# Optimization experiments

Measured on AMD Instinct MI355X. Metric: run time of the kernel, lower is better.

## Reference

```python
import jax, jax.numpy as jnp
import numpy as np

B, S, V, D, H, L, FF = 2, 1024, 32000, 512, 8, 4, 2048
DK = D // H
WIN, GLOB = 128, 16
EPS = 1e-5


def setup_inputs() -> dict:
    key = jax.random.key(0)
    ks = jax.random.split(key, 12)
    def rn(k, shape, s=0.02):
        return jax.random.normal(k, shape, jnp.float32) * s
    ln2 = jnp.stack([jnp.ones((L, 2, D)), jnp.zeros((L, 2, D))], axis=2)   # [L, 2 norms, (scale,bias), D]
    ln3 = jnp.stack([jnp.ones((L, 3, D)), jnp.zeros((L, 3, D))], axis=2)   # [L, 3 norms, (scale,bias), D]
    fln = jnp.stack([jnp.ones((D,)), jnp.zeros((D,))], axis=0)             # [(scale,bias), D]
    return {
        "src": jax.random.randint(ks[0], (B, S), 0, V),
        "tgt": jax.random.randint(ks[1], (B, S), 0, V),
        "enc_embed": rn(ks[2], (V, D)),
        "dec_embed": rn(ks[3], (V, D)),
        "enc_attn_w": rn(ks[4], (L, 4, D, D)),   # q,k,v,o projections
        "enc_attn_b": jnp.zeros((L, 4, D)),
        "enc_ln": ln2,
        "enc_ffn_w1": rn(ks[5], (L, D, FF)),
        "enc_ffn_b1": jnp.zeros((L, FF)),
        "enc_ffn_w2": rn(ks[6], (L, FF, D)),
        "enc_ffn_b2": jnp.zeros((L, D)),
        "enc_final_ln": fln,
        "dec_attn_w": rn(ks[7], (L, 8, D, D)),   # self q,k,v,o then cross q,k,v,o
        "dec_attn_b": jnp.zeros((L, 8, D)),
        "dec_ln": ln3,
        "dec_ffn_w1": rn(ks[8], (L, D, FF)),
        "dec_ffn_b1": jnp.zeros((L, FF)),
        "dec_ffn_w2": rn(ks[9], (L, FF, D)),
        "dec_ffn_b2": jnp.zeros((L, D)),
        "dec_final_ln": fln,
        "out_w": rn(ks[10], (D, V)),
        "out_b": jnp.zeros((V,)),
    }


def _ln(x, p):
    m = jnp.mean(x, -1, keepdims=True)
    v = jnp.var(x, -1, keepdims=True)
    return p[0] * (x - m) * jax.lax.rsqrt(v + EPS) + p[1]


def _rope(x):
    # x: [B, H, S, DK]; half-split rotary embedding
    half = DK // 2
    pos = jnp.arange(x.shape[2], dtype=jnp.float32)
    inv = 1.0 / (10000.0 ** (jnp.arange(half, dtype=jnp.float32) / half))
    ang = pos[:, None] * inv[None, :]                   # [S, half]
    c, s = jnp.cos(ang), jnp.sin(ang)
    x1, x2 = x[..., :half], x[..., half:]
    return jnp.concatenate([x1 * c - x2 * s, x1 * s + x2 * c], axis=-1)


def _mask(n, causal):
    # local sliding window + global tokens, optional causal
    i = jnp.arange(n)[:, None]
    j = jnp.arange(n)[None, :]
    allowed = jnp.abs(i - j) <= WIN
    allowed = allowed | (i < GLOB) | (j < GLOB)
    if causal:
        allowed = allowed & (j <= i)
    return allowed


def _attn(q_in, k_in, v_in, w, b, causal):
    # w: [4, D, D] (q,k,v,o), b: [4, D]
    def heads(x, idx):
        y = x @ w[idx] + b[idx]
        return y.reshape(x.shape[0], x.shape[1], H, DK).transpose(0, 2, 1, 3)  # [B,H,S,DK]
    Q, K, Vh = heads(q_in, 0), heads(k_in, 1), heads(v_in, 2)
    Q, K = _rope(Q), _rope(K)
    scores = jnp.einsum('bhqd,bhkd->bhqk', Q, K) / np.sqrt(DK).astype(np.float32)
    scores = jnp.where(_mask(q_in.shape[1], causal)[None, None], scores, -1e9)
    A = jax.nn.softmax(scores, axis=-1)
    o = jnp.einsum('bhqk,bhkd->bhqd', A, Vh).transpose(0, 2, 1, 3).reshape(q_in.shape[0], q_in.shape[1], D)
    return o @ w[3] + b[3]


def _ffn(x, w1, b1, w2, b2):
    return jax.nn.gelu(x @ w1 + b1) @ w2 + b2


def _forward(src, tgt, enc_embed, dec_embed, enc_attn_w, enc_attn_b, enc_ln,
             enc_ffn_w1, enc_ffn_b1, enc_ffn_w2, enc_ffn_b2, enc_final_ln,
             dec_attn_w, dec_attn_b, dec_ln, dec_ffn_w1, dec_ffn_b1,
             dec_ffn_w2, dec_ffn_b2, dec_final_ln, out_w, out_b):
    sqrt_d = np.sqrt(D).astype(np.float32)
    # encoder
    x = enc_embed[src] * sqrt_d
    for l in range(L):
        n = _ln(x, enc_ln[l, 0])
        x = x + _attn(n, n, n, enc_attn_w[l], enc_attn_b[l], False)
        n = _ln(x, enc_ln[l, 1])
        x = x + _ffn(n, enc_ffn_w1[l], enc_ffn_b1[l], enc_ffn_w2[l], enc_ffn_b2[l])
    mem = _ln(x, enc_final_ln)
    # decoder
    y = dec_embed[tgt] * sqrt_d
    for l in range(L):
        n = _ln(y, dec_ln[l, 0])
        y = y + _attn(n, n, n, dec_attn_w[l, :4], dec_attn_b[l, :4], True)
        n = _ln(y, dec_ln[l, 1])
        y = y + _attn(n, mem, mem, dec_attn_w[l, 4:], dec_attn_b[l, 4:], False)
        n = _ln(y, dec_ln[l, 2])
        y = y + _ffn(n, dec_ffn_w1[l], dec_ffn_b1[l], dec_ffn_w2[l], dec_ffn_b2[l])
    y = _ln(y, dec_final_ln)
    return y @ out_w + out_b


def reference(src, tgt, enc_embed, dec_embed, enc_attn_w, enc_attn_b, enc_ln,
              enc_ffn_w1, enc_ffn_b1, enc_ffn_w2, enc_ffn_b2, enc_final_ln,
              dec_attn_w, dec_attn_b, dec_ln, dec_ffn_w1, dec_ffn_b1,
              dec_ffn_w2, dec_ffn_b2, dec_final_ln, out_w, out_b):
    return _forward(src, tgt, enc_embed, dec_embed, enc_attn_w, enc_attn_b, enc_ln,
                    enc_ffn_w1, enc_ffn_b1, enc_ffn_w2, enc_ffn_b2, enc_final_ln,
                    dec_attn_w, dec_attn_b, dec_ln, dec_ffn_w1, dec_ffn_b1,
                    dec_ffn_w2, dec_ffn_b2, dec_final_ln, out_w, out_b)
```

## Files before the change

kernel.cpp:

```cpp
#include <hip/hip_runtime.h>
#include <cstdint>
#include <cstddef>

#define S_LEN 1024
#define DM 512
#define NHEAD 8
#define HDIM 64
#define NLAYER 4
#define FFD 2048
#define VOC 32000
#define WINSZ 128
#define GLOBSZ 16

using half8 = __attribute__((ext_vector_type(8))) _Float16;
using f32x4 = __attribute__((ext_vector_type(4))) float;

static __device__ __forceinline__ f32x4 mfma16(half8 a, half8 b, f32x4 c) {
  return __builtin_amdgcn_mfma_f32_16x16x32_f16(a, b, c, 0, 0, 0);
}

typedef __attribute__((address_space(1))) const void gvoid;
typedef __attribute__((address_space(3))) void lvoid;
static __device__ __forceinline__ void gload16(const void* g, void* l) {
  __builtin_amdgcn_global_load_lds((gvoid*)g, (lvoid*)l, 16, 0, 0);
}
template <int N>
static __device__ __forceinline__ void waitv() {
  asm volatile("s_waitcnt vmcnt(%0)" :: "i"(N) : "memory");
}

__global__ __launch_bounds__(256) void transpose_k(const float* __restrict__ in,
                                                   _Float16* __restrict__ out,
                                                   int R, int C)
{
  __shared__ float t[32][33];
  const float* ip = in + (size_t)blockIdx.z * R * C;
  _Float16* op = out + (size_t)blockIdx.z * R * C;
  int c0 = blockIdx.x * 32, r0 = blockIdx.y * 32;
  int tx = threadIdx.x & 31, ty = threadIdx.x >> 5;
#pragma unroll
  for (int i = 0; i < 32; i += 8)
    t[ty + i][tx] = ip[(size_t)(r0 + ty + i) * C + c0 + tx];
  __syncthreads();
#pragma unroll
  for (int i = 0; i < 32; i += 8)
    op[(size_t)(c0 + ty + i) * R + r0 + tx] = (_Float16)t[tx][ty + i];
}

__global__ __launch_bounds__(256) void embed2_k(const int* __restrict__ src,
                                                const int* __restrict__ tgt,
                                                const float* __restrict__ enc_embed,
                                                const float* __restrict__ dec_embed,
                                                const float* __restrict__ enc_ln0,
                                                const float* __restrict__ dec_ln0,
                                                float* __restrict__ xbuf,
                                                float* __restrict__ ybuf,
                                                _Float16* __restrict__ nbuf,
                                                _Float16* __restrict__ nbuf2)
{
  int which = blockIdx.y;
  const int* ids = which ? tgt : src;
  const float* emb = which ? dec_embed : enc_embed;
  const float* gamma = which ? dec_ln0 : enc_ln0;
  const float* beta = gamma + 512;
  float* xout = which ? ybuf : xbuf;
  _Float16* nout = which ? nbuf2 : nbuf;

  int row = blockIdx.x * 4 + (threadIdx.x >> 6);
  int lane = threadIdx.x & 63;
  const float* er = emb + (size_t)ids[row] * DM + lane * 8;
  float4 v0 = *(const float4*)er;
  float4 v1 = *(const float4*)(er + 4);
  float vals[8] = {v0.x, v0.y, v0.z, v0.w, v1.x, v1.y, v1.z, v1.w};
  float s = 0.f, ss = 0.f;
#pragma unroll
  for (int j = 0; j < 8; ++j) {
    vals[j] *= 22.627416997969522f;
    s += vals[j]; ss += vals[j] * vals[j];
  }
#pragma unroll
  for (int m = 1; m < 64; m <<= 1) { s += __shfl_xor(s, m); ss += __shfl_xor(ss, m); }
  float mean = s * (1.f / 512.f);
  float var = ss * (1.f / 512.f) - mean * mean;
  float rstd = rsqrtf(var + 1e-5f);
  float* xr = xout + (size_t)row * DM + lane * 8;
  _Float16* orow = nout + (size_t)row * DM + lane * 8;
  const float* gp = gamma + lane * 8;
  const float* bp = beta + lane * 8;
#pragma unroll
  for (int j = 0; j < 8; ++j) {
    xr[j] = vals[j];
    orow[j] = (_Float16)(gp[j] * (vals[j] - mean) * rstd + bp[j]);
  }
}

__global__ __launch_bounds__(256) void ln_k(const float* __restrict__ x,
                                            const float* __restrict__ gamma,
                                            const float* __restrict__ beta,
                                            _Float16* __restrict__ outp)
{
  int row = blockIdx.x * 4 + (threadIdx.x >> 6);
  int lane = threadIdx.x & 63;
  const float* xr = x + (size_t)row * DM + lane * 8;
  float4 v0 = *(const float4*)xr;
  float4 v1 = *(const float4*)(xr + 4);
  float vals[8] = {v0.x, v0.y, v0.z, v0.w, v1.x, v1.y, v1.z, v1.w};
  float s = 0.f, ss = 0.f;
#pragma unroll
  for (int j = 0; j < 8; ++j) { s += vals[j]; ss += vals[j] * vals[j]; }
#pragma unroll
  for (int m = 1; m < 64; m <<= 1) { s += __shfl_xor(s, m); ss += __shfl_xor(ss, m); }
  float mean = s * (1.f / 512.f);
  float var = ss * (1.f / 512.f) - mean * mean;
  float rstd = rsqrtf(var + 1e-5f);
  _Float16* orow = outp + (size_t)row * DM + lane * 8;
  const float* gp = gamma + lane * 8;
  const float* bp = beta + lane * 8;
#pragma unroll
  for (int j = 0; j < 8; ++j)
    orow[j] = (_Float16)(gp[j] * (vals[j] - mean) * rstd + bp[j]);
}

template <int BM, int BN, int EPI, int MODE, bool WIDE = (MODE != 0)>
__global__ __launch_bounds__(256) void gemm_k(const _Float16* __restrict__ A,
                                              const _Float16* __restrict__ B,
                                              const float* __restrict__ bias,
                                              const float* __restrict__ resid,
                                              void* __restrict__ Cout,
                                              _Float16* __restrict__ vtout,
                                              int M, int N, int K)
{
  constexpr int WAVE_M = WIDE ? BM / 4 : BM / 2;
  constexpr int WAVE_N = WIDE ? BN : BN / 2;
  constexpr int FMW = WAVE_M / 16;
  constexpr int FNW = WAVE_N / 16;
  constexpr int LPS = BM / 32 + BN / 32;
  static_assert(MODE == 0 || (WIDE && BN == 64), "rope modes need 64-col waves");

  __shared__ __align__(16) _Float16 As[3][BM * 64];
  __shared__ __align__(16) _Float16 Bs[3][BN * 64];
  const int tid = threadIdx.x;
  const int lane = tid & 63, wid = tid >> 6;
  const int g = lane >> 4, ql = lane & 15;

  const int gx = gridDim.x;
  const int nwg = gx * gridDim.y;
  const int orig = blockIdx.y * gx + blockIdx.x;
  const int q = nwg >> 3, r = nwg & 7;
  const int xcd = orig & 7, rest = orig >> 3;
  const int id = (xcd < r ? xcd * (q + 1) : r * (q + 1) + (xcd - r) * q) + rest;
  const int bm = (id % gx) * BM, bn = (id / gx) * BN;
  const int wm = WIDE ? wid * WAVE_M : (wid >> 1) * WAVE_M;
  const int wn = WIDE ? 0 : (wid & 1) * WAVE_N;

  const _Float16* Bp;
  if constexpr (MODE == 2) {
    int srcrow0 = ((bn >> 10) * 8 + 5 + ((bn >> 9) & 1)) * 512 + (bn & 511);
    Bp = B + (size_t)srcrow0 * K;
  } else {
    Bp = B + (size_t)bn * K;
  }

  f32x4 acc[FMW][FNW];
#pragma unroll
  for (int a = 0; a < FMW; ++a)
#pragma unroll
    for (int b = 0; b < FNW; ++b) acc[a][b] = f32x4{0.f, 0.f, 0.f, 0.f};

  auto stage = [&](int buf, int kt) {
#pragma unroll
    for (int r2 = 0; r2 < BM / 32; ++r2) {
      int off = r2 * 4096 + tid * 16;
      int row = off >> 7, slot = (off >> 4) & 7;
      gload16(A + (size_t)(bm + row) * K + kt + ((slot ^ (row & 7)) << 3),
              (char*)&As[buf][0] + r2 * 4096 + wid * 1024);
    }
#pragma unroll
    for (int r2 = 0; r2 < BN / 32; ++r2) {
      int off = r2 * 4096 + tid * 16;
      int row = off >> 7, slot = (off >> 4) & 7;
      gload16(Bp + (size_t)row * K + kt + ((slot ^ (row & 7)) << 3),
              (char*)&Bs[buf][0] + r2 * 4096 + wid * 1024);
    }
  };

  auto compute = [&](int cur) {
#pragma unroll
    for (int kk = 0; kk < 2; ++kk) {
      half8 af[FMW], bf[FNW];
#pragma unroll
      for (int a = 0; a < FMW; ++a) {
        int row = wm + a * 16 + ql;
        af[a] = *(const half8*)((const char*)&As[cur][0] + row * 128 + (((kk * 4 + g) ^ (row & 7)) << 4));
      }
#pragma unroll
      for (int b = 0; b < FNW; ++b) {
        int row = wn + b * 16 + ql;
        bf[b] = *(const half8*)((const char*)&Bs[cur][0] + row * 128 + (((kk * 4 + g) ^ (row & 7)) << 4));
      }
      __builtin_amdgcn_s_setprio(1);
#pragma unroll
      for (int a = 0; a < FMW; ++a)
#pragma unroll
        for (int b = 0; b < FNW; ++b) acc[a][b] = mfma16(af[a], bf[b], acc[a][b]);
      __builtin_amdgcn_s_setprio(0);
    }
  };

  const int nk = K >> 6;
  stage(0, 0);
  stage(1, 64);
  for (int t = 0; t < nk; ++t) {
    if (t + 1 < nk) waitv<LPS>(); else waitv<0>();
    __builtin_amdgcn_s_barrier();
    __builtin_amdgcn_sched_barrier(0);
    if (t + 2 < nk) stage((t + 2) % 3, (t + 2) << 6);
    compute(t % 3);
  }

#pragma unroll
  for (int a = 0; a < FMW; ++a) {
    const int row0 = bm + wm + a * 16 + g * 4;
    float v[FNW][4];
#pragma unroll
    for (int b2 = 0; b2 < FNW; ++b2) {
      int col = bn + wn + b2 * 16 + ql;
      float bv;
      if constexpr (MODE == 2) {
        int bcol = ((col >> 10) * 8 + 5 + ((col >> 9) & 1)) * 512 + (col & 511);
        bv = bias[bcol];
      } else {
        bv = bias[col];
      }
#pragma unroll
      for (int r2 = 0; r2 < 4; ++r2) v[b2][r2] = acc[a][b2][r2] + bv;
    }
    if constexpr (MODE != 0) {
      const int seg = bn >> 9;
      bool dorope = (MODE == 3) || (MODE == 1 && seg < 2) ||
                    (MODE == 2 && ((bn >> 9) & 1) == 0);
      if (dorope) {
        const float scale = (MODE == 3 || (MODE == 1 && seg == 0)) ? 0.125f : 1.0f;
#pragma unroll
        for (int b2 = 0; b2 < 2; ++b2) {
          int d = b2 * 16 + ql;
          float inv = __expf(-(float)d * 0.28782313662425574f);
#pragma unroll
          for (int r2 = 0; r2 < 4; ++r2) {
            float sp = (float)((row0 & 1023) + r2);
            float sn, cs; __sincosf(sp * inv, &sn, &cs);
            float x1 = v[b2][r2], x2 = v[b2 + 2][r2];
            v[b2][r2]     = (x1 * cs - x2 * sn) * scale;
            v[b2 + 2][r2] = (x1 * sn + x2 * cs) * scale;
          }
        }
      }
    }
#pragma unroll
    for (int b2 = 0; b2 < FNW; ++b2) {
      int col = bn + wn + b2 * 16 + ql;
      if constexpr (MODE == 1) {
        if (col < 1024) {
#pragma unroll
          for (int r2 = 0; r2 < 4; ++r2)
            ((_Float16*)Cout)[(size_t)(row0 + r2) * 1024 + col] = (_Float16)v[b2][r2];
        } else {
          int rowidx = ((row0 >> 10) << 9) + (col - 1024);
          union { _Float16 h[4]; uint2 u; } pk;
#pragma unroll
          for (int r2 = 0; r2 < 4; ++r2) pk.h[r2] = (_Float16)v[b2][r2];
          *(uint2*)&vtout[((size_t)rowidx << 10) + (row0 & 1023)] = pk.u;
        }
      } else if constexpr (MODE == 2) {
        if ((col & 1023) < 512) {
#pragma unroll
          for (int r2 = 0; r2 < 4; ++r2)
            ((_Float16*)Cout)[(size_t)(row0 + r2) * 2048 + ((col >> 10) << 9) + (col & 511)] = (_Float16)v[b2][r2];
        } else {
          int rowidx = (col & ~1023) + ((row0 >> 10) << 9) + (col & 511);
          union { _Float16 h[4]; uint2 u; } pk;
#pragma unroll
          for (int r2 = 0; r2 < 4; ++r2) pk.h[r2] = (_Float16)v[b2][r2];
          *(uint2*)&vtout[((size_t)rowidx << 10) + (row0 & 1023)] = pk.u;
        }
      } else {
#pragma unroll
        for (int r2 = 0; r2 < 4; ++r2) {
          float x = v[b2][r2];
          if constexpr (EPI == 1) {
            float u = x;
            x = u / (1.f + __expf(-1.5957691216057308f * (u + 0.044715f * u * u * u)));
          }
          if constexpr (EPI == 2) x += resid[(size_t)(row0 + r2) * N + col];
          if constexpr (EPI == 0 || EPI == 1)
            ((_Float16*)Cout)[(size_t)(row0 + r2) * N + col] = (_Float16)x;
          else if constexpr (EPI == 2)
            ((float*)Cout)[(size_t)(row0 + r2) * N + col] = x;
          else
            __builtin_nontemporal_store(x, &((float*)Cout)[(size_t)(row0 + r2) * N + col]);
        }
      }
    }
  }
}

template <bool CAUSAL>
__global__ __launch_bounds__(256) void attn_k(const _Float16* __restrict__ qb, int qs, int qoff,
                                              const _Float16* __restrict__ kb, int ks, int koff,
                                              const _Float16* __restrict__ vt,
                                              _Float16* __restrict__ out)
{
  __shared__ _Float16 plds[4][16 * 40];
  const int bh = blockIdx.y, b = bh >> 3, h = bh & 7;
  const int wid = threadIdx.x >> 6, lane = threadIdx.x & 63;
  const int g = lane >> 4, ql = lane & 15;
  const int q0 = blockIdx.x * 64 + wid * 16;
  const size_t rb = (size_t)b * S_LEN;

  half8 qf0, qf1;
  {
    const _Float16* qp = qb + (rb + q0 + ql) * qs + qoff + h * HDIM + g * 8;
    qf0 = *(const half8*)qp;
    qf1 = *(const half8*)(qp + 32);
  }
  float mrun[4] = {-1e30f, -1e30f, -1e30f, -1e30f};
  float srun[4] = {0.f, 0.f, 0.f, 0.f};
  f32x4 oacc[4];
#pragma unroll
  for (int c = 0; c < 4; ++c) oacc[c] = f32x4{0.f, 0.f, 0.f, 0.f};

  const _Float16* vbase = vt + (((size_t)(b * 512 + h * HDIM)) << 10);
  _Float16* pw = plds[wid];

  auto proc = [&](int k0) {
    const _Float16* kp = kb + (rb + k0 + ql) * ks + koff + h * HDIM + g * 8;
    half8 kf00 = *(const half8*)kp;
    half8 kf01 = *(const half8*)(kp + 32);
    half8 kf10 = *(const half8*)(kp + (size_t)16 * ks);
    half8 kf11 = *(const half8*)(kp + (size_t)16 * ks + 32);

    f32x4 s0 = f32x4{0.f, 0.f, 0.f, 0.f};
    f32x4 s1 = f32x4{0.f, 0.f, 0.f, 0.f};
    __builtin_amdgcn_s_setprio(1);
    s0 = mfma16(qf0, kf00, s0); s0 = mfma16(qf1, kf01, s0);
    s1 = mfma16(qf0, kf10, s1); s1 = mfma16(qf1, kf11, s1);
    __builtin_amdgcn_s_setprio(0);

    float p0[4], p1[4];
#pragma unroll
    for (int r = 0; r < 4; ++r) {
      int i = q0 + 4 * g + r;
      int j0 = k0 + ql, j1 = j0 + 16;
      float a0 = s0[r], a1 = s1[r];
      int d0 = i - j0, d1 = i - j1;
      bool ok0 = (d0 <= WINSZ && d0 >= -WINSZ) || (i < GLOBSZ) || (j0 < GLOBSZ);
      bool ok1 = (d1 <= WINSZ && d1 >= -WINSZ) || (i < GLOBSZ) || (j1 < GLOBSZ);
      if (CAUSAL) { ok0 = ok0 && (j0 <= i); ok1 = ok1 && (j1 <= i); }
      a0 = ok0 ? a0 : -1e9f;
      a1 = ok1 ? a1 : -1e9f;
      float mx = fmaxf(a0, a1);
      mx = fmaxf(mx, __shfl_xor(mx, 1));
      mx = fmaxf(mx, __shfl_xor(mx, 2));
      mx = fmaxf(mx, __shfl_xor(mx, 4));
      mx = fmaxf(mx, __shfl_xor(mx, 8));
      float mnew = fmaxf(mrun[r], mx);
      float alpha = __expf(mrun[r] - mnew);
      float e0 = __expf(a0 - mnew), e1 = __expf(a1 - mnew);
      float ps = e0 + e1;
      ps += __shfl_xor(ps, 1);
      ps += __shfl_xor(ps, 2);
      ps += __shfl_xor(ps, 4);
      ps += __shfl_xor(ps, 8);
      srun[r] = srun[r] * alpha + ps;
      mrun[r] = mnew;
#pragma unroll
      for (int c = 0; c < 4; ++c) oacc[c][r] *= alpha;
      p0[r] = e0; p1[r] = e1;
    }
#pragma unroll
    for (int r = 0; r < 4; ++r) {
      pw[(4 * g + r) * 40 + ql] = (_Float16)p0[r];
      pw[(4 * g + r) * 40 + 16 + ql] = (_Float16)p1[r];
    }
    half8 pa = *(const half8*)&pw[ql * 40 + g * 8];
    __builtin_amdgcn_s_setprio(1);
#pragma unroll
    for (int c = 0; c < 4; ++c) {
      half8 vf = *(const half8*)(vbase + (((size_t)(16 * c + ql)) << 10) + k0 + 8 * g);
      oacc[c] = mfma16(pa, vf, oacc[c]);
    }
    __builtin_amdgcn_s_setprio(0);
  };

  const int kend = CAUSAL ? (q0 + 16) : S_LEN;
  int lo = 0, hi = kend;
  if (q0 >= GLOBSZ) {
    lo = (q0 - WINSZ) & ~31;
    if (lo < 0) lo = 0;
    if (!CAUSAL) {
      int h2 = q0 + 16 + WINSZ;
      hi = (h2 < kend) ? h2 : kend;
    }
  }
  if (lo > 0) proc(0);
  for (int k0 = lo; k0 < hi; k0 += 32) proc(k0);

#pragma unroll
  for (int c = 0; c < 4; ++c)
#pragma unroll
    for (int r = 0; r < 4; ++r) {
      float val = oacc[c][r] / srun[r];
      out[(rb + q0 + 4 * g + r) * DM + h * HDIM + 16 * c + ql] = (_Float16)val;
    }
}

extern "C" void kernel_launch(void* const* d_in, const int* in_sizes, int n_in,
                              void* d_out, int out_size, void* d_ws, size_t ws_size,
                              hipStream_t stream)
{
  const int*   src         = (const int*)d_in[0];
  const int*   tgt         = (const int*)d_in[1];
  const float* enc_embed   = (const float*)d_in[2];
  const float* dec_embed   = (const float*)d_in[3];
  const float* enc_attn_w  = (const float*)d_in[4];
  const float* enc_attn_b  = (const float*)d_in[5];
  const float* enc_ln      = (const float*)d_in[6];
  const float* enc_ffn_w1  = (const float*)d_in[7];
  const float* enc_ffn_b1  = (const float*)d_in[8];
  const float* enc_ffn_w2  = (const float*)d_in[9];
  const float* enc_ffn_b2  = (const float*)d_in[10];
  const float* enc_fln     = (const float*)d_in[11];
  const float* dec_attn_w  = (const float*)d_in[12];
  const float* dec_attn_b  = (const float*)d_in[13];
  const float* dec_ln      = (const float*)d_in[14];
  const float* dec_ffn_w1  = (const float*)d_in[15];
  const float* dec_ffn_b1  = (const float*)d_in[16];
  const float* dec_ffn_w2  = (const float*)d_in[17];
  const float* dec_ffn_b2  = (const float*)d_in[18];
  const float* dec_fln     = (const float*)d_in[19];
  const float* out_w       = (const float*)d_in[20];
  const float* out_b       = (const float*)d_in[21];
  float* logits = (float*)d_out;

  char* wsp = (char*)d_ws;
  size_t off = 0;
  auto alloc = [&](size_t bytes) -> void* {
    void* p = wsp + off;
    off += (bytes + 255) & ~(size_t)255;
    return p;
  };
  _Float16* enc_attn_wt = (_Float16*)alloc((size_t)16 * 512 * 512 * 2);
  _Float16* dec_attn_wt = (_Float16*)alloc((size_t)32 * 512 * 512 * 2);
  _Float16* e_ffn1_wt   = (_Float16*)alloc((size_t)4 * 2048 * 512 * 2);
  _Float16* e_ffn2_wt   = (_Float16*)alloc((size_t)4 * 2048 * 512 * 2);
  _Float16* d_ffn1_wt   = (_Float16*)alloc((size_t)4 * 2048 * 512 * 2);
  _Float16* d_ffn2_wt   = (_Float16*)alloc((size_t)4 * 2048 * 512 * 2);
  _Float16* out_wt      = (_Float16*)alloc((size_t)VOC * 512 * 2);
  float*    xbuf        = (float*)alloc((size_t)2048 * 512 * 4);
  float*    ybuf        = (float*)alloc((size_t)2048 * 512 * 4);
  _Float16* nbuf        = (_Float16*)alloc((size_t)2048 * 512 * 2);
  _Float16* nbuf2       = (_Float16*)alloc((size_t)2048 * 512 * 2);
  _Float16* qkvb        = (_Float16*)alloc((size_t)2048 * 1024 * 2);
  _Float16* aob         = (_Float16*)alloc((size_t)2048 * 512 * 2);
  _Float16* hbuf        = (_Float16*)alloc((size_t)2048 * 2048 * 2);
  _Float16* memb        = (_Float16*)alloc((size_t)2048 * 512 * 2);
  _Float16* cqb         = (_Float16*)alloc((size_t)2048 * 512 * 2);
  _Float16* ckvb        = (_Float16*)alloc((size_t)2048 * 2048 * 2);
  _Float16* vts         = (_Float16*)alloc((size_t)2 * 512 * 1024 * 2);
  _Float16* vtc         = (_Float16*)alloc((size_t)8 * 512 * 1024 * 2);

  transpose_k<<<dim3(16, 16, 16), 256, 0, stream>>>(enc_attn_w, enc_attn_wt, 512, 512);
  transpose_k<<<dim3(16, 16, 32), 256, 0, stream>>>(dec_attn_w, dec_attn_wt, 512, 512);
  transpose_k<<<dim3(64, 16, 4), 256, 0, stream>>>(enc_ffn_w1, e_ffn1_wt, 512, 2048);
  transpose_k<<<dim3(16, 64, 4), 256, 0, stream>>>(enc_ffn_w2, e_ffn2_wt, 2048, 512);
  transpose_k<<<dim3(64, 16, 4), 256, 0, stream>>>(dec_ffn_w1, d_ffn1_wt, 512, 2048);
  transpose_k<<<dim3(16, 64, 4), 256, 0, stream>>>(dec_ffn_w2, d_ffn2_wt, 2048, 512);
  transpose_k<<<dim3(1000, 16, 1), 256, 0, stream>>>(out_w, out_wt, 512, VOC);

  embed2_k<<<dim3(512, 2), 256, 0, stream>>>(src, tgt, enc_embed, dec_embed,
                                             enc_ln, dec_ln, xbuf, ybuf, nbuf, nbuf2);

  for (int l = 0; l < NLAYER; ++l) {
    const float* g0 = enc_ln + ((size_t)(l * 2 + 0) * 2 + 0) * 512;
    if (l > 0) ln_k<<<512, 256, 0, stream>>>(xbuf, g0, g0 + 512, nbuf);
    gemm_k<64, 64, 0, 1><<<dim3(32, 24), 256, 0, stream>>>(
        nbuf, enc_attn_wt + (size_t)l * 4 * 262144,
        enc_attn_b + (size_t)l * 4 * 512, nullptr, qkvb, vts, 2048, 1536, 512);
    attn_k<false><<<dim3(16, 16), 256, 0, stream>>>(qkvb, 1024, 0, qkvb, 1024, 512, vts, aob);
    gemm_k<64, 32, 2, 0><<<dim3(32, 16), 256, 0, stream>>>(
        aob, enc_attn_wt + (size_t)(l * 4 + 3) * 262144,
        enc_attn_b + (size_t)(l * 4 + 3) * 512, xbuf, xbuf, nullptr, 2048, 512, 512);
    const float* g1 = enc_ln + ((size_t)(l * 2 + 1) * 2 + 0) * 512;
    ln_k<<<512, 256, 0, stream>>>(xbuf, g1, g1 + 512, nbuf);
    gemm_k<64, 64, 1, 0><<<dim3(32, 32), 256, 0, stream>>>(
        nbuf, e_ffn1_wt + (size_t)l * 2048 * 512,
        enc_ffn_b1 + (size_t)l * 2048, nullptr, hbuf, nullptr, 2048, 2048, 512);
    gemm_k<64, 32, 2, 0><<<dim3(32, 16), 256, 0, stream>>>(
        hbuf, e_ffn2_wt + (size_t)l * 512 * 2048,
        enc_ffn_b2 + (size_t)l * 512, xbuf, xbuf, nullptr, 2048, 512, 2048);
  }
  ln_k<<<512, 256, 0, stream>>>(xbuf, enc_fln, enc_fln + 512, memb);

  gemm_k<64, 64, 0, 2><<<dim3(32, 64), 256, 0, stream>>>(
      memb, dec_attn_wt, dec_attn_b, nullptr, ckvb, vtc, 2048, 4096, 512);

  for (int l = 0; l < NLAYER; ++l) {
    const float* g0 = dec_ln + ((size_t)(l * 3 + 0) * 2 + 0) * 512;
    const _Float16* dn = (l == 0) ? nbuf2 : nbuf;
    if (l > 0) ln_k<<<512, 256, 0, stream>>>(ybuf, g0, g0 + 512, nbuf);
    gemm_k<64, 64, 0, 1><<<dim3(32, 24), 256, 0, stream>>>(
        dn, dec_attn_wt + (size_t)l * 8 * 262144,
        dec_attn_b + (size_t)l * 8 * 512, nullptr, qkvb, vts, 2048, 1536, 512);
    attn_k<true><<<dim3(16, 16), 256, 0, stream>>>(qkvb, 1024, 0, qkvb, 1024, 512, vts, aob);
    gemm_k<64, 32, 2, 0><<<dim3(32, 16), 256, 0, stream>>>(
        aob, dec_attn_wt + (size_t)(l * 8 + 3) * 262144,
        dec_attn_b + (size_t)(l * 8 + 3) * 512, ybuf, ybuf, nullptr, 2048, 512, 512);
    const float* g1 = dec_ln + ((size_t)(l * 3 + 1) * 2 + 0) * 512;
    ln_k<<<512, 256, 0, stream>>>(ybuf, g1, g1 + 512, nbuf);
    gemm_k<64, 64, 0, 3><<<dim3(32, 8), 256, 0, stream>>>(
        nbuf, dec_attn_wt + (size_t)(l * 8 + 4) * 262144,
        dec_attn_b + (size_t)(l * 8 + 4) * 512, nullptr, cqb, nullptr, 2048, 512, 512);
    attn_k<false><<<dim3(16, 16), 256, 0, stream>>>(cqb, 512, 0, ckvb, 2048, l * 512,
                                                    vtc + ((size_t)l << 20), aob);
    gemm_k<64, 32, 2, 0><<<dim3(32, 16), 256, 0, stream>>>(
        aob, dec_attn_wt + (size_t)(l * 8 + 7) * 262144,
        dec_attn_b + (size_t)(l * 8 + 7) * 512, ybuf, ybuf, nullptr, 2048, 512, 512);
    const float* g2 = dec_ln + ((size_t)(l * 3 + 2) * 2 + 0) * 512;
    ln_k<<<512, 256, 0, stream>>>(ybuf, g2, g2 + 512, nbuf);
    gemm_k<64, 64, 1, 0><<<dim3(32, 32), 256, 0, stream>>>(
        nbuf, d_ffn1_wt + (size_t)l * 2048 * 512,
        dec_ffn_b1 + (size_t)l * 2048, nullptr, hbuf, nullptr, 2048, 2048, 512);
    gemm_k<64, 32, 2, 0><<<dim3(32, 16), 256, 0, stream>>>(
        hbuf, d_ffn2_wt + (size_t)l * 512 * 2048,
        dec_ffn_b2 + (size_t)l * 512, ybuf, ybuf, nullptr, 2048, 512, 2048);
  }

  ln_k<<<512, 256, 0, stream>>>(ybuf, dec_fln, dec_fln + 512, nbuf);
  gemm_k<128, 64, 3, 0><<<dim3(16, 500), 256, 0, stream>>>(
      nbuf, out_wt, out_b, nullptr, logits, nullptr, 2048, VOC, 512);
}
```

Baseline: 1.203 ms.

## Merge weight transposes, retune GEMM swizzle/scheduling, and halve attention block size

```diff
diff --git a/kernel.cpp b/kernel.cpp
--- a/kernel.cpp
+++ b/kernel.cpp
@@ -29,13 +29,18 @@
   asm volatile("s_waitcnt vmcnt(%0)" :: "i"(N) : "memory");
 }
 
-__global__ __launch_bounds__(256) void transpose_k(const float* __restrict__ in,
-                                                   _Float16* __restrict__ out,
-                                                   int R, int C)
+__global__ __launch_bounds__(256) void transpose2_k(const float* __restrict__ inA,
+                                                    const float* __restrict__ inB,
+                                                    _Float16* __restrict__ outA,
+                                                    _Float16* __restrict__ outB,
+                                                    int R, int C, int splitZ)
 {
   __shared__ float t[32][33];
-  const float* ip = in + (size_t)blockIdx.z * R * C;
-  _Float16* op = out + (size_t)blockIdx.z * R * C;
+  int z = blockIdx.z;
+  const float* ip;
+  _Float16* op;
+  if (z < splitZ) { ip = inA + (size_t)z * R * C; op = outA + (size_t)z * R * C; }
+  else { ip = inB + (size_t)(z - splitZ) * R * C; op = outB + (size_t)(z - splitZ) * R * C; }
   int c0 = blockIdx.x * 32, r0 = blockIdx.y * 32;
   int tx = threadIdx.x & 31, ty = threadIdx.x >> 5;
 #pragma unroll
@@ -121,7 +126,7 @@
     orow[j] = (_Float16)(gp[j] * (vals[j] - mean) * rstd + bp[j]);
 }
 
-template <int BM, int BN, int EPI, int MODE, bool WIDE = (MODE != 0)>
+template <int BM, int BN, int EPI, int MODE, bool SWZ = false, bool NT = false>
 __global__ __launch_bounds__(256) void gemm_k(const _Float16* __restrict__ A,
                                               const _Float16* __restrict__ B,
                                               const float* __restrict__ bias,
@@ -130,10 +135,11 @@
                                               _Float16* __restrict__ vtout,
                                               int M, int N, int K)
 {
+  constexpr bool WIDE = (BN >= 64);
   constexpr int WAVE_M = WIDE ? BM / 4 : BM / 2;
   constexpr int WAVE_N = WIDE ? BN : BN / 2;
   constexpr int FMW = WAVE_M / 16;
-  constexpr int FNW = WAVE_N / 16;
+  constexpr int FNW = WIDE ? BN / 16 : BN / 32;
   constexpr int LPS = BM / 32 + BN / 32;
   static_assert(MODE == 0 || (WIDE && BN == 64), "rope modes need 64-col waves");
 
@@ -143,13 +149,18 @@
   const int lane = tid & 63, wid = tid >> 6;
   const int g = lane >> 4, ql = lane & 15;
 
-  const int gx = gridDim.x;
-  const int nwg = gx * gridDim.y;
-  const int orig = blockIdx.y * gx + blockIdx.x;
-  const int q = nwg >> 3, r = nwg & 7;
-  const int xcd = orig & 7, rest = orig >> 3;
-  const int id = (xcd < r ? xcd * (q + 1) : r * (q + 1) + (xcd - r) * q) + rest;
-  const int bm = (id % gx) * BM, bn = (id / gx) * BN;
+  int bm, bn;
+  if constexpr (SWZ) {
+    const int gx = gridDim.x;
+    const int nwg = gx * gridDim.y;
+    const int orig = blockIdx.y * gx + blockIdx.x;
+    const int q = nwg >> 3, r = nwg & 7;
+    const int xcd = orig & 7, rest = orig >> 3;
+    const int id = (xcd < r ? xcd * (q + 1) : r * (q + 1) + (xcd - r) * q) + rest;
+    bm = (id % gx) * BM; bn = (id / gx) * BN;
+  } else {
+    bm = blockIdx.x * BM; bn = blockIdx.y * BN;
+  }
   const int wm = WIDE ? wid * WAVE_M : (wid >> 1) * WAVE_M;
   const int wn = WIDE ? 0 : (wid & 1) * WAVE_N;
 
@@ -198,12 +209,10 @@
         int row = wn + b * 16 + ql;
         bf[b] = *(const half8*)((const char*)&Bs[cur][0] + row * 128 + (((kk * 4 + g) ^ (row & 7)) << 4));
       }
-      __builtin_amdgcn_s_setprio(1);
 #pragma unroll
       for (int a = 0; a < FMW; ++a)
 #pragma unroll
         for (int b = 0; b < FNW; ++b) acc[a][b] = mfma16(af[a], bf[b], acc[a][b]);
-      __builtin_amdgcn_s_setprio(0);
     }
   };
 
@@ -214,8 +223,8 @@
     if (t + 1 < nk) waitv<LPS>(); else waitv<0>();
     __builtin_amdgcn_s_barrier();
     __builtin_amdgcn_sched_barrier(0);
+    compute(t % 3);
     if (t + 2 < nk) stage((t + 2) % 3, (t + 2) << 6);
-    compute(t % 3);
   }
 
 #pragma unroll
@@ -294,10 +303,10 @@
           if constexpr (EPI == 2) x += resid[(size_t)(row0 + r2) * N + col];
           if constexpr (EPI == 0 || EPI == 1)
             ((_Float16*)Cout)[(size_t)(row0 + r2) * N + col] = (_Float16)x;
-          else if constexpr (EPI == 2)
+          else if constexpr (NT)
+            __builtin_nontemporal_store(x, &((float*)Cout)[(size_t)(row0 + r2) * N + col]);
+          else
             ((float*)Cout)[(size_t)(row0 + r2) * N + col] = x;
-          else
-            __builtin_nontemporal_store(x, &((float*)Cout)[(size_t)(row0 + r2) * N + col]);
         }
       }
     }
@@ -305,16 +314,16 @@
 }
 
 template <bool CAUSAL>
-__global__ __launch_bounds__(256) void attn_k(const _Float16* __restrict__ qb, int qs, int qoff,
+__global__ __launch_bounds__(128) void attn_k(const _Float16* __restrict__ qb, int qs, int qoff,
                                               const _Float16* __restrict__ kb, int ks, int koff,
                                               const _Float16* __restrict__ vt,
                                               _Float16* __restrict__ out)
 {
-  __shared__ _Float16 plds[4][16 * 40];
+  __shared__ _Float16 plds[2][16 * 40];
   const int bh = blockIdx.y, b = bh >> 3, h = bh & 7;
   const int wid = threadIdx.x >> 6, lane = threadIdx.x & 63;
   const int g = lane >> 4, ql = lane & 15;
-  const int q0 = blockIdx.x * 64 + wid * 16;
+  const int q0 = blockIdx.x * 32 + wid * 16;
   const size_t rb = (size_t)b * S_LEN;
 
   half8 qf0, qf1;
@@ -341,10 +350,8 @@
 
     f32x4 s0 = f32x4{0.f, 0.f, 0.f, 0.f};
     f32x4 s1 = f32x4{0.f, 0.f, 0.f, 0.f};
-    __builtin_amdgcn_s_setprio(1);
     s0 = mfma16(qf0, kf00, s0); s0 = mfma16(qf1, kf01, s0);
     s1 = mfma16(qf0, kf10, s1); s1 = mfma16(qf1, kf11, s1);
-    __builtin_amdgcn_s_setprio(0);
 
     float p0[4], p1[4];
 #pragma unroll
@@ -383,13 +390,11 @@
       pw[(4 * g + r) * 40 + 16 + ql] = (_Float16)p1[r];
     }
     half8 pa = *(const half8*)&pw[ql * 40 + g * 8];
-    __builtin_amdgcn_s_setprio(1);
 #pragma unroll
     for (int c = 0; c < 4; ++c) {
       half8 vf = *(const half8*)(vbase + (((size_t)(16 * c + ql)) << 10) + k0 + 8 * g);
       oacc[c] = mfma16(pa, vf, oacc[c]);
     }
-    __builtin_amdgcn_s_setprio(0);
   };
 
   const int kend = CAUSAL ? (q0 + 16) : S_LEN;
@@ -469,13 +474,13 @@
   _Float16* vts         = (_Float16*)alloc((size_t)2 * 512 * 1024 * 2);
   _Float16* vtc         = (_Float16*)alloc((size_t)8 * 512 * 1024 * 2);
 
-  transpose_k<<<dim3(16, 16, 16), 256, 0, stream>>>(enc_attn_w, enc_attn_wt, 512, 512);
-  transpose_k<<<dim3(16, 16, 32), 256, 0, stream>>>(dec_attn_w, dec_attn_wt, 512, 512);
-  transpose_k<<<dim3(64, 16, 4), 256, 0, stream>>>(enc_ffn_w1, e_ffn1_wt, 512, 2048);
-  transpose_k<<<dim3(16, 64, 4), 256, 0, stream>>>(enc_ffn_w2, e_ffn2_wt, 2048, 512);
-  transpose_k<<<dim3(64, 16, 4), 256, 0, stream>>>(dec_ffn_w1, d_ffn1_wt, 512, 2048);
-  transpose_k<<<dim3(16, 64, 4), 256, 0, stream>>>(dec_ffn_w2, d_ffn2_wt, 2048, 512);
-  transpose_k<<<dim3(1000, 16, 1), 256, 0, stream>>>(out_w, out_wt, 512, VOC);
+  transpose2_k<<<dim3(16, 16, 48), 256, 0, stream>>>(enc_attn_w, dec_attn_w,
+                                                     enc_attn_wt, dec_attn_wt, 512, 512, 16);
+  transpose2_k<<<dim3(64, 16, 8), 256, 0, stream>>>(enc_ffn_w1, dec_ffn_w1,
+                                                    e_ffn1_wt, d_ffn1_wt, 512, 2048, 4);
+  transpose2_k<<<dim3(16, 64, 8), 256, 0, stream>>>(enc_ffn_w2, dec_ffn_w2,
+                                                    e_ffn2_wt, d_ffn2_wt, 2048, 512, 4);
+  transpose2_k<<<dim3(1000, 16, 1), 256, 0, stream>>>(out_w, out_w, out_wt, out_wt, 512, VOC, 1);
 
   embed2_k<<<dim3(512, 2), 256, 0, stream>>>(src, tgt, enc_embed, dec_embed,
                                              enc_ln, dec_ln, xbuf, ybuf, nbuf, nbuf2);
@@ -486,7 +491,7 @@
     gemm_k<64, 64, 0, 1><<<dim3(32, 24), 256, 0, stream>>>(
         nbuf, enc_attn_wt + (size_t)l * 4 * 262144,
         enc_attn_b + (size_t)l * 4 * 512, nullptr, qkvb, vts, 2048, 1536, 512);
-    attn_k<false><<<dim3(16, 16), 256, 0, stream>>>(qkvb, 1024, 0, qkvb, 1024, 512, vts, aob);
+    attn_k<false><<<dim3(32, 16), 128, 0, stream>>>(qkvb, 1024, 0, qkvb, 1024, 512, vts, aob);
     gemm_k<64, 32, 2, 0><<<dim3(32, 16), 256, 0, stream>>>(
         aob, enc_attn_wt + (size_t)(l * 4 + 3) * 262144,
         enc_attn_b + (size_t)(l * 4 + 3) * 512, xbuf, xbuf, nullptr, 2048, 512, 512);
@@ -511,7 +516,7 @@
     gemm_k<64, 64, 0, 1><<<dim3(32, 24), 256, 0, stream>>>(
         dn, dec_attn_wt + (size_t)l * 8 * 262144,
         dec_attn_b + (size_t)l * 8 * 512, nullptr, qkvb, vts, 2048, 1536, 512);
-    attn_k<true><<<dim3(16, 16), 256, 0, stream>>>(qkvb, 1024, 0, qkvb, 1024, 512, vts, aob);
+    attn_k<true><<<dim3(32, 16), 128, 0, stream>>>(qkvb, 1024, 0, qkvb, 1024, 512, vts, aob);
     gemm_k<64, 32, 2, 0><<<dim3(32, 16), 256, 0, stream>>>(
         aob, dec_attn_wt + (size_t)(l * 8 + 3) * 262144,
         dec_attn_b + (size_t)(l * 8 + 3) * 512, ybuf, ybuf, nullptr, 2048, 512, 512);
@@ -520,7 +525,7 @@
     gemm_k<64, 64, 0, 3><<<dim3(32, 8), 256, 0, stream>>>(
         nbuf, dec_attn_wt + (size_t)(l * 8 + 4) * 262144,
         dec_attn_b + (size_t)(l * 8 + 4) * 512, nullptr, cqb, nullptr, 2048, 512, 512);
-    attn_k<false><<<dim3(16, 16), 256, 0, stream>>>(cqb, 512, 0, ckvb, 2048, l * 512,
+    attn_k<false><<<dim3(32, 16), 128, 0, stream>>>(cqb, 512, 0, ckvb, 2048, l * 512,
                                                     vtc + ((size_t)l << 20), aob);
     gemm_k<64, 32, 2, 0><<<dim3(32, 16), 256, 0, stream>>>(
         aob, dec_attn_wt + (size_t)(l * 8 + 7) * 262144,
@@ -536,6 +541,6 @@
   }
 
   ln_k<<<512, 256, 0, stream>>>(ybuf, dec_fln, dec_fln + 512, nbuf);
-  gemm_k<128, 64, 3, 0><<<dim3(16, 500), 256, 0, stream>>>(
+  gemm_k<128, 64, 3, 0, true, true><<<dim3(16, 500), 256, 0, stream>>>(
       nbuf, out_wt, out_b, nullptr, logits, nullptr, 2048, VOC, 512);
 }
```

New measurement: 976.0 us. 1.23x faster.
